# Kernel tuning notes

Measured on AMD Instinct MI355X. Metric: run time of the kernel, lower is better.

## Reference

```python
import jax, jax.numpy as jnp
import numpy as np

EPS = 1e-6        # module eps added to softplus(sigma)
BALL_EPS = 1e-5   # clip margin for Poincare ball projection


def _norm(x):
    return jnp.sqrt(jnp.clip(jnp.sum(x * x, axis=-1, keepdims=True), 1e-15))


def _clip_norm(x, max_norm):
    n = _norm(x)
    return x * jnp.minimum(1.0, max_norm / n)


def _artanh(x):
    return jnp.arctanh(jnp.clip(x, -1.0 + 1e-7, 1.0 - 1e-7))


def _expmap0(u, c):
    """pre_clip -> PoincareBall.expmap0 -> post_clip."""
    sc = jnp.sqrt(c)
    max_tan = jnp.arctanh(jnp.asarray(1.0 - BALL_EPS, u.dtype)) / sc
    u = _clip_norm(u, max_tan)                      # pre_clip on tangent norm
    n = _norm(u)
    y = jnp.tanh(sc * n) * u / (sc * n)
    return _clip_norm(y, (1.0 - BALL_EPS) / sc)     # post_clip inside ball


def _logmap0(y, c):
    sc = jnp.sqrt(c)
    n = _norm(y)
    return _artanh(sc * n) * y / (sc * n)


def _pair_dist(qh, kh, c):
    """Poincare distance d(q_i, k_j) computed from inner products (no [B,H,N,J,D] tensor).
    qh: (B,H,N,D), kh: (B,H,J,D) -> (B,H,N,J).
    d = (2/sqrt(c)) * artanh(sqrt(c) * ||(-q) mobius_add k||).
    """
    x2 = jnp.sum(qh * qh, -1)[..., :, None]   # (B,H,N,1)
    y2 = jnp.sum(kh * kh, -1)[..., None, :]   # (B,H,1,J)
    xy = jnp.einsum('bhnd,bhjd->bhnj', qh, kh)
    A = 1.0 - 2.0 * c * xy + c * y2
    Bc = 1.0 - c * x2
    num2 = A * A * x2 - 2.0 * A * Bc * xy + Bc * Bc * y2   # ||numerator||^2
    den = 1.0 - 2.0 * c * xy + (c * c) * x2 * y2
    arg = jnp.sqrt(c) * jnp.sqrt(jnp.clip(num2, 0.0)) / jnp.clip(den, 1e-15)
    return (2.0 / jnp.sqrt(c)) * _artanh(arg)


def _mobius_scalar_mul(r, x, c):
    sc = jnp.sqrt(c)
    n = _norm(x)
    return jnp.tanh(r * _artanh(sc * n)) * x / (sc * n)


def setup_inputs() -> dict:
    key = jax.random.key(0)
    ks = jax.random.split(key, 8)
    B, N, D, H, M = 16, 576, 768, 12, 128
    Hd = D // H
    std = 0.02
    isp1 = float(np.log(np.expm1(1.0)))  # inv_softplus(1.0)
    return {
        'x': jax.random.normal(ks[0], (B, N, D), jnp.float32),
        'Wq': jax.random.normal(ks[1], (D, D), jnp.float32) * std,
        'bq': jnp.zeros((D,), jnp.float32),
        'Wk': jax.random.normal(ks[2], (D, D), jnp.float32) * std,
        'bk': jnp.zeros((D,), jnp.float32),
        'Wv': jax.random.normal(ks[3], (D, D), jnp.float32) * std,
        'bv': jnp.zeros((D,), jnp.float32),
        'Wo': jax.random.normal(ks[4], (D, D), jnp.float32) * std,
        'bo': jnp.zeros((D,), jnp.float32),
        'centroids': jax.random.normal(ks[5], (H, M, Hd), jnp.float32) * std,
        'curv_raw': jnp.full((1,), isp1, jnp.float32),
        'sigma_raw': jnp.full((H,), isp1, jnp.float32),
    }


def reference(x, Wq, bq, Wk, bk, Wv, bv, Wo, bo, centroids, curv_raw, sigma_raw):
    B, N, D = x.shape
    H, M, Hd = centroids.shape
    c = jax.nn.softplus(curv_raw[0])

    def split(t):  # (B,N,D) -> (B,H,N,Hd)
        return t.reshape(B, N, H, Hd).transpose(0, 2, 1, 3)

    q = split(x @ Wq.T + bq)
    k = split(x @ Wk.T + bk)
    v = split(x @ Wv.T + bv)

    Cb = jnp.broadcast_to(centroids[None], (B, H, M, Hd))
    K_aug = jnp.concatenate([k, Cb], axis=2)   # (B,H,J,Hd), J = N + M
    V_aug = jnp.concatenate([v, Cb], axis=2)

    q_h = _expmap0(q, c)
    K_h = _expmap0(K_aug, c)
    V_h = _expmap0(V_aug, c)

    d = _pair_dist(q_h, K_h, c)                              # (B,H,N,J)
    sigma = (jax.nn.softplus(sigma_raw) + EPS)[None, :, None, None]
    W = jax.nn.softmax(-(d * d) / (2.0 * sigma * sigma), axis=-1)

    # Riemannian weighted midpoint (geoopt weighted_midpoint with k=-c):
    # gamma = lambda_x = 2 / (1 - c||x||^2)
    gamma = 2.0 / jnp.clip(1.0 - c * jnp.sum(V_h * V_h, -1), 1e-15)  # (B,H,J)
    nom = jnp.einsum('bhnj,bhjd->bhnd', W * gamma[:, :, None, :], V_h)
    den = jnp.einsum('bhnj,bhj->bhn', W, gamma - 1.0)
    den = jnp.where(den >= 0, jnp.maximum(den, 1e-10), jnp.minimum(den, -1e-10))
    two_mean = nom / den[..., None]
    O_h = _mobius_scalar_mul(0.5, two_mean, c)
    O_euc = _logmap0(O_h, c)                                  # (B,H,N,Hd)

    out = O_euc.transpose(0, 2, 1, 3).reshape(B, N, H * Hd)
    return out @ Wo.T + bo
```

## Files before the change

### kernel.cpp

```cpp
#include <hip/hip_runtime.h>
#include <cstdint>
#include <cstddef>

#define B_  16
#define N_  576
#define D_  768
#define H_  12
#define HD_ 64
#define M_  128
#define J_  704

typedef unsigned short u16;
typedef __attribute__((ext_vector_type(8))) short bf16x8;
typedef __attribute__((ext_vector_type(4))) float f32x4;
typedef __attribute__((ext_vector_type(4))) unsigned short u16x4;
typedef __attribute__((ext_vector_type(8))) unsigned short u16x8;


__device__ __forceinline__ float softplus_f(float x) {
    return (x > 20.f) ? x : log1pf(expf(x));
}

__device__ __forceinline__ float wred_sum64(float v) {
#pragma unroll
    for (int m = 1; m < 64; m <<= 1) v += __shfl_xor(v, m, 64);
    return v;
}

__device__ __forceinline__ u16 bf16_rne(float f) {
    unsigned int u = __float_as_uint(f);
    unsigned int r = u + 0x7FFFu + ((u >> 16) & 1u);
    return (u16)(r >> 16);
}
__device__ __forceinline__ float bf16_tof(u16 h) {
    return __uint_as_float(((unsigned int)h) << 16);
}

__device__ __forceinline__ float expmap0_factor(float n2, float sc, float* n2out) {
    const float ATANH_1M1E5 = 6.1030335f;
    float n0 = sqrtf(fmaxf(n2, 1e-15f));
    float maxtan = ATANH_1M1E5 / sc;
    float f1 = fminf(1.f, maxtan / n0);
    float n1 = n0 * f1;
    float a  = sc * n1;
    float th = tanhf(a);
    float yfac  = th / a;
    float ynorm = th / sc;
    float lim   = (1.f - 1e-5f) / sc;
    float f2 = fminf(1.f, lim / ynorm);
    float fn = ynorm * f2;
    *n2out = fn * fn;
    return f1 * yfac * f2;
}

__device__ __forceinline__ float artanh_fast(float z) {
    return 0.5f * __logf((1.f + z) / (1.f - z));
}

typedef const __attribute__((address_space(1))) unsigned int* gas_u32;
typedef __attribute__((address_space(3))) unsigned int* las_u32;
__device__ __forceinline__ void gload_lds16(const u16* g, u16* l) {
    __builtin_amdgcn_global_load_lds((gas_u32)(const void*)g, (las_u32)(void*)l, 16, 0, 0);
}

__global__ __launch_bounds__(256) void split_bf16_kernel(
    const float* __restrict__ src, u16* __restrict__ hi, u16* __restrict__ lo, int n4)
{
    int i = blockIdx.x * 256 + threadIdx.x;
    if (i >= n4) return;
    float4 v = ((const float4*)src)[i];
    u16x4 h, l;
    h[0] = bf16_rne(v.x); l[0] = bf16_rne(v.x - bf16_tof(h[0]));
    h[1] = bf16_rne(v.y); l[1] = bf16_rne(v.y - bf16_tof(h[1]));
    h[2] = bf16_rne(v.z); l[2] = bf16_rne(v.z - bf16_tof(h[2]));
    h[3] = bf16_rne(v.w); l[3] = bf16_rne(v.w - bf16_tof(h[3]));
    ((u16x4*)hi)[i] = h;
    ((u16x4*)lo)[i] = l;
}

__global__ __launch_bounds__(256) void split_w4_kernel(
    const float* __restrict__ W0, const float* __restrict__ W1,
    const float* __restrict__ W2, const float* __restrict__ W3,
    u16* __restrict__ H0, u16* __restrict__ L0, u16* __restrict__ H1, u16* __restrict__ L1,
    u16* __restrict__ H2, u16* __restrict__ L2, u16* __restrict__ H3, u16* __restrict__ L3)
{
    int i = blockIdx.x * 256 + threadIdx.x;
    const int wsel = blockIdx.y;
    const float* src = wsel == 0 ? W0 : (wsel == 1 ? W1 : (wsel == 2 ? W2 : W3));
    u16* hi = wsel == 0 ? H0 : (wsel == 1 ? H1 : (wsel == 2 ? H2 : H3));
    u16* lo = wsel == 0 ? L0 : (wsel == 1 ? L1 : (wsel == 2 ? L2 : L3));
    float4 v = ((const float4*)src)[i];
    u16x4 h, l;
    h[0] = bf16_rne(v.x); l[0] = bf16_rne(v.x - bf16_tof(h[0]));
    h[1] = bf16_rne(v.y); l[1] = bf16_rne(v.y - bf16_tof(h[1]));
    h[2] = bf16_rne(v.z); l[2] = bf16_rne(v.z - bf16_tof(h[2]));
    h[3] = bf16_rne(v.w); l[3] = bf16_rne(v.w - bf16_tof(h[3]));
    ((u16x4*)hi)[i] = h;
    ((u16x4*)lo)[i] = l;
}

__global__ __launch_bounds__(256) void gemm_qkv_mfma(
    const u16* __restrict__ xh, const u16* __restrict__ xl,
    const u16* __restrict__ Wh0, const u16* __restrict__ Wl0,
    const u16* __restrict__ Wh1, const u16* __restrict__ Wl1,
    const u16* __restrict__ Wh2, const u16* __restrict__ Wl2,
    const float* __restrict__ bq, const float* __restrict__ bk, const float* __restrict__ bv,
    float* __restrict__ qh_o, float* __restrict__ Kh_o, float* __restrict__ Vh_o)
{
    __shared__ u16 Ah[4096], Al[4096], Bh[4096], Bl[4096];
    const int tid = threadIdx.x;
    const int w = tid >> 6, lane = tid & 63;
    const int wr = w >> 1, wc = w & 1;
    const int lrow = lane & 15, lk8 = (lane >> 4) << 3;
    const int bid = blockIdx.x;
    const int xcd = bid & 7, ser = bid >> 3;
    const int mt = xcd * 9 + (ser % 9);
    const int yb = ser / 9;
    const int which = yb / 6, ct = yb - which * 6;
    const u16* Bp_h = which == 0 ? Wh0 : (which == 1 ? Wh1 : Wh2);
    const u16* Bp_l = which == 0 ? Wl0 : (which == 1 ? Wl1 : Wl2);
    const int row0 = mt * 128, col0 = ct * 128;

    const size_t a0 = (size_t)(row0 + (2 * w + 0) * 16 + lrow) * 768 + lk8;
    const size_t a1 = a0 + 16 * 768;
    const size_t b0 = (size_t)(col0 + (2 * w + 0) * 16 + lrow) * 768 + lk8;
    const size_t b1 = b0 + 16 * 768;
    u16* lAh0 = Ah + (2 * w) * 512; u16* lAh1 = lAh0 + 512;
    u16* lAl0 = Al + (2 * w) * 512; u16* lAl1 = lAl0 + 512;
    u16* lBh0 = Bh + (2 * w) * 512; u16* lBh1 = lBh0 + 512;
    u16* lBl0 = Bl + (2 * w) * 512; u16* lBl1 = lBl0 + 512;

    f32x4 acc[4][4];
#pragma unroll
    for (int i = 0; i < 4; ++i)
#pragma unroll
        for (int j = 0; j < 4; ++j) acc[i][j] = (f32x4){0.f, 0.f, 0.f, 0.f};

    for (int k0 = 0; k0 < 768; k0 += 32) {
        gload_lds16(xh + a0 + k0, lAh0);
        gload_lds16(xh + a1 + k0, lAh1);
        gload_lds16(xl + a0 + k0, lAl0);
        gload_lds16(xl + a1 + k0, lAl1);
        gload_lds16(Bp_h + b0 + k0, lBh0);
        gload_lds16(Bp_h + b1 + k0, lBh1);
        gload_lds16(Bp_l + b0 + k0, lBl0);
        gload_lds16(Bp_l + b1 + k0, lBl1);
        __syncthreads();
        bf16x8 aH[4], aL[4], bH[4], bL[4];
        const int lo8 = lane * 8;
#pragma unroll
        for (int i = 0; i < 4; ++i) {
            aH[i] = *(const bf16x8*)(Ah + (wr * 4 + i) * 512 + lo8);
            aL[i] = *(const bf16x8*)(Al + (wr * 4 + i) * 512 + lo8);
            bH[i] = *(const bf16x8*)(Bh + (wc * 4 + i) * 512 + lo8);
            bL[i] = *(const bf16x8*)(Bl + (wc * 4 + i) * 512 + lo8);
        }
#pragma unroll
        for (int mi = 0; mi < 4; ++mi)
#pragma unroll
            for (int ni = 0; ni < 4; ++ni) {
                acc[mi][ni] = __builtin_amdgcn_mfma_f32_16x16x32_bf16(aH[mi], bH[ni], acc[mi][ni], 0, 0, 0);
                acc[mi][ni] = __builtin_amdgcn_mfma_f32_16x16x32_bf16(aH[mi], bL[ni], acc[mi][ni], 0, 0, 0);
                acc[mi][ni] = __builtin_amdgcn_mfma_f32_16x16x32_bf16(aL[mi], bH[ni], acc[mi][ni], 0, 0, 0);
            }
        __syncthreads();
    }

    const float* bias = which == 0 ? bq : (which == 1 ? bk : bv);
    const int h = ct * 2 + wc;
    const int rbase = row0 + wr * 64 + ((lane >> 4) << 2);
#pragma unroll
    for (int ni = 0; ni < 4; ++ni) {
        const int hd = ni * 16 + lrow;
        const float bv_ = bias[h * 64 + hd];
#pragma unroll
        for (int mi = 0; mi < 4; ++mi) {
            f32x4 a = acc[mi][ni];
#pragma unroll
            for (int r = 0; r < 4; ++r) {
                int row = rbase + mi * 16 + r;
                int bb = row / 576;
                int nn = row - bb * 576;
                float val = a[r] + bv_;
                size_t dst = (((size_t)(bb * 12 + h)) * 576 + nn) * 64 + hd;
                if (which == 0)      qh_o[dst] = val;
                else if (which == 1) Kh_o[dst] = val;
                else                 Vh_o[dst] = val;
            }
        }
    }
}

__global__ __launch_bounds__(256) void gemm_o_mfma(
    const u16* __restrict__ Oh, const u16* __restrict__ Ol,
    const u16* __restrict__ Wh, const u16* __restrict__ Wl,
    const float* __restrict__ bo, float* __restrict__ out)
{
    __shared__ u16 Ah[4096], Al[4096], Bh[4096], Bl[4096];
    const int tid = threadIdx.x;
    const int w = tid >> 6, lane = tid & 63;
    const int wr = w >> 1, wc = w & 1;
    const int lrow = lane & 15, lk8 = (lane >> 4) << 3;
    const int bid = blockIdx.x;
    const int xcd = bid & 7, ser = bid >> 3;
    const int mt = xcd * 9 + (ser % 9);
    const int ct = ser / 9;
    const int row0 = mt * 128, col0 = ct * 128;

    const size_t a0 = (size_t)(row0 + (2 * w + 0) * 16 + lrow) * 768 + lk8;
    const size_t a1 = a0 + 16 * 768;
    const size_t b0 = (size_t)(col0 + (2 * w + 0) * 16 + lrow) * 768 + lk8;
    const size_t b1 = b0 + 16 * 768;
    u16* lAh0 = Ah + (2 * w) * 512; u16* lAh1 = lAh0 + 512;
    u16* lAl0 = Al + (2 * w) * 512; u16* lAl1 = lAl0 + 512;
    u16* lBh0 = Bh + (2 * w) * 512; u16* lBh1 = lBh0 + 512;
    u16* lBl0 = Bl + (2 * w) * 512; u16* lBl1 = lBl0 + 512;

    f32x4 acc[4][4];
#pragma unroll
    for (int i = 0; i < 4; ++i)
#pragma unroll
        for (int j = 0; j < 4; ++j) acc[i][j] = (f32x4){0.f, 0.f, 0.f, 0.f};

    for (int k0 = 0; k0 < 768; k0 += 32) {
        gload_lds16(Oh + a0 + k0, lAh0);
        gload_lds16(Oh + a1 + k0, lAh1);
        gload_lds16(Ol + a0 + k0, lAl0);
        gload_lds16(Ol + a1 + k0, lAl1);
        gload_lds16(Wh + b0 + k0, lBh0);
        gload_lds16(Wh + b1 + k0, lBh1);
        gload_lds16(Wl + b0 + k0, lBl0);
        gload_lds16(Wl + b1 + k0, lBl1);
        __syncthreads();
        bf16x8 aH[4], aL[4], bH[4], bL[4];
        const int lo8 = lane * 8;
#pragma unroll
        for (int i = 0; i < 4; ++i) {
            aH[i] = *(const bf16x8*)(Ah + (wr * 4 + i) * 512 + lo8);
            aL[i] = *(const bf16x8*)(Al + (wr * 4 + i) * 512 + lo8);
            bH[i] = *(const bf16x8*)(Bh + (wc * 4 + i) * 512 + lo8);
            bL[i] = *(const bf16x8*)(Bl + (wc * 4 + i) * 512 + lo8);
        }
#pragma unroll
        for (int mi = 0; mi < 4; ++mi)
#pragma unroll
            for (int ni = 0; ni < 4; ++ni) {
                acc[mi][ni] = __builtin_amdgcn_mfma_f32_16x16x32_bf16(aH[mi], bH[ni], acc[mi][ni], 0, 0, 0);
                acc[mi][ni] = __builtin_amdgcn_mfma_f32_16x16x32_bf16(aH[mi], bL[ni], acc[mi][ni], 0, 0, 0);
                acc[mi][ni] = __builtin_amdgcn_mfma_f32_16x16x32_bf16(aL[mi], bH[ni], acc[mi][ni], 0, 0, 0);
            }
        __syncthreads();
    }

    const int rbase = row0 + wr * 64 + ((lane >> 4) << 2);
#pragma unroll
    for (int ni = 0; ni < 4; ++ni) {
        const int colg = col0 + wc * 64 + ni * 16 + lrow;
        const float bv_ = bo[colg];
#pragma unroll
        for (int mi = 0; mi < 4; ++mi) {
            f32x4 a = acc[mi][ni];
#pragma unroll
            for (int r = 0; r < 4; ++r) {
                int row = rbase + mi * 16 + r;
                out[(size_t)row * 768 + colg] = a[r] + bv_;
            }
        }
    }
}

__global__ __launch_bounds__(256) void maps_kernel(
    const float* __restrict__ qh, const float* __restrict__ Khf, const float* __restrict__ Vhf,
    const float* __restrict__ cent,
    u16* __restrict__ Qb0, u16* __restrict__ Qb1, u16* __restrict__ Qb2,
    u16* __restrict__ Kb0, u16* __restrict__ Kb1, u16* __restrict__ Kb2,
    u16* __restrict__ Kc0, u16* __restrict__ Kc1, u16* __restrict__ Kc2,
    u16* __restrict__ gV0, u16* __restrict__ gV1,
    u16* __restrict__ gVc0, u16* __restrict__ gVc1,
    float* __restrict__ x2q, float* __restrict__ y2g, float* __restrict__ gm1,
    float* __restrict__ y2c, float* __restrict__ gm1c,
    const float* __restrict__ curv_raw)
{
    __shared__ float gvt_s[64][65];
    const float c  = softplus_f(curv_raw[0]);
    const float sc = sqrtf(c);
    const int bx = blockIdx.x;
    const int w = threadIdx.x >> 6, lane = threadIdx.x & 63;

    if (bx < 1728) {
        const size_t base = (size_t)bx * 64;
#pragma unroll 4
        for (int i = 0; i < 16; ++i) {
            const size_t row = base + w * 16 + i;
            const size_t off = row * 64 + lane;
            float u = qh[off];
            float n2 = wred_sum64(u * u);
            float n2o;
            float f = expmap0_factor(n2, sc, &n2o);
            float y = u * f;
            u16 h_ = bf16_rne(y);
            float r1 = y - bf16_tof(h_);
            u16 m_ = bf16_rne(r1);
            u16 l_ = bf16_rne(r1 - bf16_tof(m_));
            Qb0[off] = h_; Qb1[off] = m_; Qb2[off] = l_;
            if (lane == 0) x2q[row] = n2o;
        }
        return;
    }
    if (bx < 3456) {
        const int t = bx - 1728;
        const int bh = t / 9, jt = t - (t / 9) * 9;
#pragma unroll 4
        for (int i = 0; i < 16; ++i) {
            const int j = jt * 64 + w * 16 + i;
            const size_t g = (size_t)bh * 576 + j;
            float kx = Khf[g * 64 + lane], vx = Vhf[g * 64 + lane];
            float n2k = wred_sum64(kx * kx);
            float n2v = wred_sum64(vx * vx);
            float y2o, v2o;
            float fk = expmap0_factor(n2k, sc, &y2o);
            float fv = expmap0_factor(n2v, sc, &v2o);
            float ky = kx * fk;
            u16 kh = bf16_rne(ky);
            float r1 = ky - bf16_tof(kh);
            u16 km = bf16_rne(r1);
            u16 kl = bf16_rne(r1 - bf16_tof(km));
            Kb0[g * 64 + lane] = kh; Kb1[g * 64 + lane] = km; Kb2[g * 64 + lane] = kl;
            float gmm = 2.f / fmaxf(1.f - c * v2o, 1e-15f);
            gvt_s[lane][w * 16 + i] = vx * fv * gmm;
            if (lane == 0) { y2g[g] = y2o; gm1[g] = gmm - 1.f; }
        }
        __syncthreads();
        const int hd = threadIdx.x >> 2, j0 = (threadIdx.x & 3) * 16;
        u16 hb[16], lb[16];
#pragma unroll
        for (int e = 0; e < 16; ++e) {
            float v = gvt_s[hd][j0 + e];
            hb[e] = bf16_rne(v);
            lb[e] = bf16_rne(v - bf16_tof(hb[e]));
        }
        const size_t dst = ((size_t)bh * 64 + hd) * 576 + jt * 64 + j0;
        *(u16x8*)(gV0 + dst)     = *(u16x8*)&hb[0];
        *(u16x8*)(gV0 + dst + 8) = *(u16x8*)&hb[8];
        *(u16x8*)(gV1 + dst)     = *(u16x8*)&lb[0];
        *(u16x8*)(gV1 + dst + 8) = *(u16x8*)&lb[8];
        return;
    }
    {
        const int t = bx - 3456;
        const int h = t >> 1, ct = t & 1;
#pragma unroll 4
        for (int i = 0; i < 16; ++i) {
            const int m = ct * 64 + w * 16 + i;
            const size_t g = (size_t)h * 128 + m;
            float cv = cent[g * 64 + lane];
            float n2 = wred_sum64(cv * cv);
            float n2o;
            float f = expmap0_factor(n2, sc, &n2o);
            float ky = cv * f;
            u16 kh = bf16_rne(ky);
            float r1 = ky - bf16_tof(kh);
            u16 km = bf16_rne(r1);
            u16 kl = bf16_rne(r1 - bf16_tof(km));
            Kc0[g * 64 + lane] = kh; Kc1[g * 64 + lane] = km; Kc2[g * 64 + lane] = kl;
            float gmm = 2.f / fmaxf(1.f - c * n2o, 1e-15f);
            gvt_s[lane][w * 16 + i] = ky * gmm;
            if (lane == 0) { y2c[g] = n2o; gm1c[g] = gmm - 1.f; }
        }
        __syncthreads();
        const int hd = threadIdx.x >> 2, j0 = (threadIdx.x & 3) * 16;
        u16 hb[16], lb[16];
#pragma unroll
        for (int e = 0; e < 16; ++e) {
            float v = gvt_s[hd][j0 + e];
            hb[e] = bf16_rne(v);
            lb[e] = bf16_rne(v - bf16_tof(hb[e]));
        }
        const size_t dst = ((size_t)h * 64 + hd) * 128 + ct * 64 + j0;
        *(u16x8*)(gVc0 + dst)     = *(u16x8*)&hb[0];
        *(u16x8*)(gVc0 + dst + 8) = *(u16x8*)&hb[8];
        *(u16x8*)(gVc1 + dst)     = *(u16x8*)&lb[0];
        *(u16x8*)(gVc1 + dst + 8) = *(u16x8*)&lb[8];
    }
}

__global__ __launch_bounds__(256) void attn_kernel(
    const u16* __restrict__ Qb0, const u16* __restrict__ Qb1, const u16* __restrict__ Qb2,
    const u16* __restrict__ Kb0, const u16* __restrict__ Kb1, const u16* __restrict__ Kb2,
    const u16* __restrict__ Kc0, const u16* __restrict__ Kc1, const u16* __restrict__ Kc2,
    const u16* __restrict__ gV0, const u16* __restrict__ gV1,
    const u16* __restrict__ gVc0, const u16* __restrict__ gVc1,
    const float* __restrict__ x2q, const float* __restrict__ y2g, const float* __restrict__ gm1,
    const float* __restrict__ y2c, const float* __restrict__ gm1c,
    const float* __restrict__ sigma_raw, const float* __restrict__ curv_raw,
    u16* __restrict__ Oh, u16* __restrict__ Ol)
{
    __shared__ __align__(16) u16 Kst[2][3][4096];
    __shared__ __align__(16) u16 Vst[2][4096];
    __shared__ __align__(16) u16 wb_hi[4][1024];
    __shared__ __align__(16) u16 wb_lo[4][1024];

    const int blk = blockIdx.x;
    const int xcd = blk & 7;
    const int serial = blk >> 3;
    const int bhg = serial / 9;
    const int qt = serial - bhg * 9;
    const int bh = bhg * 8 + xcd;
    const int b = bh / 12, h = bh % 12;
    const float c  = softplus_f(curv_raw[0]);
    const float sc = sqrtf(c);
    const float sig = softplus_f(sigma_raw[h]) + 1e-6f;
    const float coef = -2.f / (c * sig * sig);
    const float c2h  = coef * 0.25f * 0.6931471805599453f;
    const float m2c  = -2.f * c;
    const float CLIP = 1.f - 1e-7f;

    const int tid = threadIdx.x;
    const int w = tid >> 6, lane = tid & 63;
    const int lr = lane & 15, lg = lane >> 4, lo8 = lg * 8;
    const int swl = (lr & 7) << 3;

    const size_t qbase = (size_t)bh * 576 + qt * 64;

    int srow[2], scol[2];
#pragma unroll
    for (int rr = 0; rr < 2; ++rr) {
        int cch = (rr * 4 + w) * 64 + lane;
        srow[rr] = cch >> 3;
        scol[rr] = ((cch & 7) ^ (srow[rr] & 7)) << 3;
    }
    const size_t kb_base = (size_t)bh * 576 * 64;
    const size_t kc_base = (size_t)h * 128 * 64;
    const size_t vb_base = (size_t)bh * 64 * 576;
    const size_t vc_base = (size_t)h * 64 * 128;

    auto stageK = [&](int t, int buf) {
        if (t < 9) {
            const size_t rb = kb_base + (size_t)t * 64 * 64;
#pragma unroll
            for (int rr = 0; rr < 2; ++rr) {
                const size_t so = rb + (size_t)srow[rr] * 64 + scol[rr];
                gload_lds16(Kb0 + so, &Kst[buf][0][(rr * 4 + w) * 512]);
                gload_lds16(Kb1 + so, &Kst[buf][1][(rr * 4 + w) * 512]);
                gload_lds16(Kb2 + so, &Kst[buf][2][(rr * 4 + w) * 512]);
            }
        } else {
            const size_t rb = kc_base + (size_t)(t - 9) * 64 * 64;
#pragma unroll
            for (int rr = 0; rr < 2; ++rr) {
                const size_t so = rb + (size_t)srow[rr] * 64 + scol[rr];
                gload_lds16(Kc0 + so, &Kst[buf][0][(rr * 4 + w) * 512]);
                gload_lds16(Kc1 + so, &Kst[buf][1][(rr * 4 + w) * 512]);
                gload_lds16(Kc2 + so, &Kst[buf][2][(rr * 4 + w) * 512]);
            }
        }
    };
    auto stageV = [&](int t) {
        if (t < 9) {
            const size_t rb = vb_base + (size_t)t * 64;
#pragma unroll
            for (int rr = 0; rr < 2; ++rr) {
                const size_t so = rb + (size_t)srow[rr] * 576 + scol[rr];
                gload_lds16(gV0 + so, &Vst[0][(rr * 4 + w) * 512]);
                gload_lds16(gV1 + so, &Vst[1][(rr * 4 + w) * 512]);
            }
        } else {
            const size_t rb = vc_base + (size_t)(t - 9) * 64;
#pragma unroll
            for (int rr = 0; rr < 2; ++rr) {
                const size_t so = rb + (size_t)srow[rr] * 128 + scol[rr];
                gload_lds16(gVc0 + so, &Vst[0][(rr * 4 + w) * 512]);
                gload_lds16(gVc1 + so, &Vst[1][(rr * 4 + w) * 512]);
            }
        }
    };

    bf16x8 aQh[2], aQm[2], aQl[2];
    {
        const size_t qrow = (qbase + w * 16 + lr) * 64;
#pragma unroll
        for (int kt = 0; kt < 2; ++kt) {
            const size_t o = qrow + kt * 32 + lo8;
            aQh[kt] = *(const bf16x8*)(Qb0 + o);
            aQm[kt] = *(const bf16x8*)(Qb1 + o);
            aQl[kt] = *(const bf16x8*)(Qb2 + o);
        }
    }
    float x2r[4], m2Bc[4], Bc2[4], ccx2[4];
#pragma unroll
    for (int r = 0; r < 4; ++r) {
        float x2 = x2q[qbase + w * 16 + lg * 4 + r];
        float Bc = fmaf(-c, x2, 1.f);
        x2r[r] = x2; m2Bc[r] = -2.f * Bc; Bc2[r] = Bc * Bc; ccx2[r] = c * c * x2;
    }

    f32x4 pv[4];
#pragma unroll
    for (int i = 0; i < 4; ++i) pv[i] = (f32x4){0.f, 0.f, 0.f, 0.f};
    float den[4] = {0.f, 0.f, 0.f, 0.f};

    u16* wbh = &wb_hi[w][0];
    u16* wbl = &wb_lo[w][0];

    stageK(0, 0);
    __syncthreads();

    int cur = 0;
    for (int jt = 0; jt < 11; ++jt) {
        const int jb = jt * 64;

        if (jt < 10) stageK(jt + 1, cur ^ 1);
        stageV(jt);

        const float* y2p;
        const float* gm1p;
        if (jt < 9) { y2p = y2g + (size_t)bh * 576 + jb;  gm1p = gm1 + (size_t)bh * 576 + jb; }
        else        { y2p = y2c + (size_t)h * 128 + (jb - 576); gm1p = gm1c + (size_t)h * 128 + (jb - 576); }

        const u16* kp0 = &Kst[cur][0][0];
        const u16* kp1 = &Kst[cur][1][0];
        const u16* kp2 = &Kst[cur][2][0];
        f32x4 sf[4];
        float y2v[4], gm1v[4];
#pragma unroll
        for (int jf = 0; jf < 4; ++jf) {
            y2v[jf] = y2p[jf * 16 + lr];
            gm1v[jf] = gm1p[jf * 16 + lr];
            const int rb = (jf * 16 + lr) * 64;
            f32x4 s = (f32x4){0.f, 0.f, 0.f, 0.f};
#pragma unroll
            for (int kt = 0; kt < 2; ++kt) {
                const int o = rb + ((kt * 32 + lo8) ^ swl);
                bf16x8 kh = *(const bf16x8*)(kp0 + o);
                bf16x8 km = *(const bf16x8*)(kp1 + o);
                bf16x8 kl = *(const bf16x8*)(kp2 + o);
                s = __builtin_amdgcn_mfma_f32_16x16x32_bf16(aQh[kt], kh, s, 0, 0, 0);
                s = __builtin_amdgcn_mfma_f32_16x16x32_bf16(aQh[kt], km, s, 0, 0, 0);
                s = __builtin_amdgcn_mfma_f32_16x16x32_bf16(aQm[kt], kh, s, 0, 0, 0);
                s = __builtin_amdgcn_mfma_f32_16x16x32_bf16(aQm[kt], km, s, 0, 0, 0);
                s = __builtin_amdgcn_mfma_f32_16x16x32_bf16(aQh[kt], kl, s, 0, 0, 0);
                s = __builtin_amdgcn_mfma_f32_16x16x32_bf16(aQl[kt], kh, s, 0, 0, 0);
            }
            sf[jf] = s;
        }

#pragma unroll
        for (int jf = 0; jf < 4; ++jf) {
            const float y2 = y2v[jf];
            const float cy2 = c * y2;
#pragma unroll
            for (int r = 0; r < 4; ++r) {
                float xy = sf[jf][r];
                float one = fmaf(m2c, xy, 1.f);
                float A   = one + cy2;
                float dn  = fmaf(ccx2[r], y2, one);
                float u   = A * x2r[r];
                u = fmaf(m2Bc[r], xy, u);
                float num2 = fmaf(A, u, Bc2[r] * y2);
                num2 = fmaxf(num2, 0.f);
                float s = sqrtf(num2) * sc;
                float dnc = fmaxf(dn, 1e-15f);
                s = fminf(s, dnc * CLIP);
                float td = __builtin_amdgcn_logf(dnc + s) - __builtin_amdgcn_logf(dnc - s);
                float wv_ = __builtin_amdgcn_exp2f(c2h * td * td);
                sf[jf][r] = wv_;
                den[r] = fmaf(wv_, gm1v[jf], den[r]);
            }
        }

#pragma unroll
        for (int r = 0; r < 4; ++r) {
            const int row = lg * 4 + r;
            const int sw = (row & 7) << 3;
#pragma unroll
            for (int jf = 0; jf < 4; ++jf) {
                const int colu = (jf * 16 + lr) ^ sw;
                float wv_ = sf[jf][r];
                u16 hb = bf16_rne(wv_);
                wbh[row * 64 + colu] = hb;
                wbl[row * 64 + colu] = bf16_rne(wv_ - bf16_tof(hb));
            }
        }

        __syncthreads();

        bf16x8 aWh[2], aWl[2];
#pragma unroll
        for (int kt = 0; kt < 2; ++kt) {
            const int colu = (kt * 32 + lo8) ^ swl;
            aWh[kt] = *(const bf16x8*)(wbh + lr * 64 + colu);
            aWl[kt] = *(const bf16x8*)(wbl + lr * 64 + colu);
        }

#pragma unroll
        for (int hf = 0; hf < 4; ++hf) {
            const int rb = (hf * 16 + lr) * 64;
#pragma unroll
            for (int kt = 0; kt < 2; ++kt) {
                const int o = rb + ((kt * 32 + lo8) ^ swl);
                bf16x8 vh = *(const bf16x8*)(&Vst[0][o]);
                bf16x8 vl = *(const bf16x8*)(&Vst[1][o]);
                pv[hf] = __builtin_amdgcn_mfma_f32_16x16x32_bf16(aWh[kt], vh, pv[hf], 0, 0, 0);
                pv[hf] = __builtin_amdgcn_mfma_f32_16x16x32_bf16(aWh[kt], vl, pv[hf], 0, 0, 0);
                pv[hf] = __builtin_amdgcn_mfma_f32_16x16x32_bf16(aWl[kt], vh, pv[hf], 0, 0, 0);
            }
        }

        __syncthreads();
        cur ^= 1;
    }

#pragma unroll
    for (int r = 0; r < 4; ++r) {
        float d = den[r];
#pragma unroll
        for (int msk = 1; msk < 16; msk <<= 1) d += __shfl_xor(d, msk, 64);
        float rd = 1.f / d;
        float o_[4];
        float n2 = 0.f;
#pragma unroll
        for (int hf = 0; hf < 4; ++hf) { o_[hf] = pv[hf][r] * rd; n2 = fmaf(o_[hf], o_[hf], n2); }
#pragma unroll
        for (int msk = 1; msk < 16; msk <<= 1) n2 += __shfl_xor(n2, msk, 64);
        float nrm = sqrtf(fmaxf(n2, 1e-15f));
        float arg = fminf(sc * nrm, 1.f - 1e-7f);
        float t = artanh_fast(arg);
        float f = 0.5f * t / (sc * nrm);
        const int nrow = qt * 64 + w * 16 + lg * 4 + r;
        const size_t dst = ((size_t)(b * 576 + nrow)) * 768 + h * 64;
#pragma unroll
        for (int hf = 0; hf < 4; ++hf) {
            float val = o_[hf] * f;
            u16 hb = bf16_rne(val);
            Oh[dst + hf * 16 + lr] = hb;
            Ol[dst + hf * 16 + lr] = bf16_rne(val - bf16_tof(hb));
        }
    }
}

extern "C" void kernel_launch(void* const* d_in, const int* in_sizes, int n_in,
                              void* d_out, int out_size, void* d_ws, size_t ws_size,
                              hipStream_t stream) {
    (void)in_sizes; (void)n_in; (void)out_size; (void)ws_size;
    const float* x    = (const float*)d_in[0];
    const float* Wq   = (const float*)d_in[1];
    const float* bq   = (const float*)d_in[2];
    const float* Wk   = (const float*)d_in[3];
    const float* bk   = (const float*)d_in[4];
    const float* Wv   = (const float*)d_in[5];
    const float* bv   = (const float*)d_in[6];
    const float* Wo   = (const float*)d_in[7];
    const float* bo   = (const float*)d_in[8];
    const float* cent = (const float*)d_in[9];
    const float* curv = (const float*)d_in[10];
    const float* sigr = (const float*)d_in[11];
    float* out = (float*)d_out;

    const size_t QH  = (size_t)B_ * H_ * N_ * 64;
    const size_t CK  = (size_t)H_ * M_ * 64;
    const size_t WSZ = (size_t)D_ * D_;

    float* fp = (float*)d_ws;
    float* qh   = fp;            fp += QH;
    float* Khf  = fp;            fp += QH;
    float* Vhf  = fp;            fp += QH;
    float* x2q  = fp;            fp += (size_t)B_ * H_ * N_;
    float* y2g  = fp;            fp += (size_t)B_ * H_ * N_;
    float* gm1  = fp;            fp += (size_t)B_ * H_ * N_;
    float* y2c  = fp;            fp += (size_t)H_ * M_;
    float* gm1c = fp;            fp += (size_t)H_ * M_;
    u16* up = (u16*)fp;
    u16* xh  = up;  up += QH;
    u16* xl  = up;  up += QH;
    u16* Oh  = xh;
    u16* Ol  = xl;
    u16* Wqh = up;  up += WSZ;
    u16* Wql = up;  up += WSZ;
    u16* Wkh = up;  up += WSZ;
    u16* Wkl = up;  up += WSZ;
    u16* Wvh = up;  up += WSZ;
    u16* Wvl = up;  up += WSZ;
    u16* Woh = up;  up += WSZ;
    u16* Wol = up;  up += WSZ;
    u16* Qb  = up;  up += 3 * QH;
    u16* Kb  = up;  up += 3 * QH;
    u16* gV  = up;  up += 2 * QH;
    u16* Kc  = up;  up += 3 * CK;
    u16* gVc = up;  up += 2 * CK;

    u16* Qb0 = Qb;           u16* Qb1 = Qb + QH;   u16* Qb2 = Qb + 2 * QH;
    u16* Kb0 = Kb;           u16* Kb1 = Kb + QH;   u16* Kb2 = Kb + 2 * QH;
    u16* gV0 = gV;           u16* gV1 = gV + QH;
    u16* Kc0 = Kc;           u16* Kc1 = Kc + CK;   u16* Kc2 = Kc + 2 * CK;
    u16* gVc0 = gVc;         u16* gVc1 = gVc + CK;

    split_bf16_kernel<<<(int)(QH / 4 / 256), 256, 0, stream>>>(x, xh, xl, (int)(QH / 4));
    split_w4_kernel<<<dim3((int)(WSZ / 4 / 256), 4), 256, 0, stream>>>(
        Wq, Wk, Wv, Wo, Wqh, Wql, Wkh, Wkl, Wvh, Wvl, Woh, Wol);

    gemm_qkv_mfma<<<1296, 256, 0, stream>>>(xh, xl, Wqh, Wql, Wkh, Wkl, Wvh, Wvl,
                                            bq, bk, bv, qh, Khf, Vhf);
    maps_kernel<<<3480, 256, 0, stream>>>(qh, Khf, Vhf, cent,
                                          Qb0, Qb1, Qb2, Kb0, Kb1, Kb2, Kc0, Kc1, Kc2,
                                          gV0, gV1, gVc0, gVc1,
                                          x2q, y2g, gm1, y2c, gm1c, curv);
    attn_kernel<<<1728, 256, 0, stream>>>(Qb0, Qb1, Qb2, Kb0, Kb1, Kb2, Kc0, Kc1, Kc2,
                                          gV0, gV1, gVc0, gVc1,
                                          x2q, y2g, gm1, y2c, gm1c, sigr, curv, Oh, Ol);
    gemm_o_mfma<<<432, 256, 0, stream>>>(Oh, Ol, Woh, Wol, bo, out);
}
```

Measured before the change: 458.7 us.

## Fuse expmap0 and bf16 splitting into QKV GEMM epilogue, drop maps kernel

The QKV GEMM epilogue now computes per-row norms with lane shuffles across the MFMA tile, applies the expmap0 factor, and writes the multi-bf16 split Q/K and gamma-scaled transposed V directly, along with the per-row scalars. This removes the fp32 q/K/V intermediates and the separate maps kernel's read/write pass. Centroid processing moves to a small standalone kernel. In exchange the epilogue does more arithmetic and issues scattered 2-byte stores for Q/K, which may be poorly coalesced.

```diff
diff --git a/kernel.cpp b/kernel.cpp
--- a/kernel.cpp
+++ b/kernel.cpp
@@ -105,7 +105,11 @@
     const u16* __restrict__ Wh1, const u16* __restrict__ Wl1,
     const u16* __restrict__ Wh2, const u16* __restrict__ Wl2,
     const float* __restrict__ bq, const float* __restrict__ bk, const float* __restrict__ bv,
-    float* __restrict__ qh_o, float* __restrict__ Kh_o, float* __restrict__ Vh_o)
+    u16* __restrict__ Qb0, u16* __restrict__ Qb1, u16* __restrict__ Qb2,
+    u16* __restrict__ Kb0, u16* __restrict__ Kb1, u16* __restrict__ Kb2,
+    u16* __restrict__ gV0, u16* __restrict__ gV1,
+    float* __restrict__ x2q, float* __restrict__ y2g, float* __restrict__ gm1,
+    const float* __restrict__ curv_raw)
 {
     __shared__ u16 Ah[4096], Al[4096], Bh[4096], Bl[4096];
     const int tid = threadIdx.x;
@@ -169,23 +173,84 @@
     const float* bias = which == 0 ? bq : (which == 1 ? bk : bv);
     const int h = ct * 2 + wc;
     const int rbase = row0 + wr * 64 + ((lane >> 4) << 2);
-#pragma unroll
-    for (int ni = 0; ni < 4; ++ni) {
-        const int hd = ni * 16 + lrow;
-        const float bv_ = bias[h * 64 + hd];
-#pragma unroll
-        for (int mi = 0; mi < 4; ++mi) {
+    const float c  = softplus_f(curv_raw[0]);
+    const float sc = sqrtf(c);
+    float bvv[4];
+#pragma unroll
+    for (int ni = 0; ni < 4; ++ni) bvv[ni] = bias[h * 64 + ni * 16 + lrow];
+
+#pragma unroll
+    for (int mi = 0; mi < 4; ++mi) {
+        float v4[4][4];
+#pragma unroll
+        for (int ni = 0; ni < 4; ++ni) {
             f32x4 a = acc[mi][ni];
 #pragma unroll
-            for (int r = 0; r < 4; ++r) {
-                int row = rbase + mi * 16 + r;
-                int bb = row / 576;
-                int nn = row - bb * 576;
-                float val = a[r] + bv_;
-                size_t dst = (((size_t)(bb * 12 + h)) * 576 + nn) * 64 + hd;
-                if (which == 0)      qh_o[dst] = val;
-                else if (which == 1) Kh_o[dst] = val;
-                else                 Vh_o[dst] = val;
+            for (int r = 0; r < 4; ++r) v4[ni][r] = a[r] + bvv[ni];
+        }
+        float f_[4], n2o_[4];
+#pragma unroll
+        for (int r = 0; r < 4; ++r) {
+            float p[4];
+#pragma unroll
+            for (int ni = 0; ni < 4; ++ni) {
+                float s = v4[ni][r] * v4[ni][r];
+#pragma unroll
+                for (int m = 1; m < 16; m <<= 1) s += __shfl_xor(s, m, 64);
+                p[ni] = s;
+            }
+            float n2 = (p[0] + p[1]) + (p[2] + p[3]);
+            f_[r] = expmap0_factor(n2, sc, &n2o_[r]);
+        }
+        const int row0g = rbase + mi * 16;
+        const int bb = row0g / 576;
+        const int nn0 = row0g - bb * 576;
+        const size_t gbase = ((size_t)(bb * 12 + h)) * 576 + nn0;
+        if (which == 2) {
+            float gmm[4];
+#pragma unroll
+            for (int r = 0; r < 4; ++r) gmm[r] = 2.f / fmaxf(1.f - c * n2o_[r], 1e-15f);
+            if (lrow == 0) {
+#pragma unroll
+                for (int r = 0; r < 4; ++r) gm1[gbase + r] = gmm[r] - 1.f;
+            }
+#pragma unroll
+            for (int ni = 0; ni < 4; ++ni) {
+                const int hd = ni * 16 + lrow;
+                u16x4 hs, ls;
+#pragma unroll
+                for (int r = 0; r < 4; ++r) {
+                    float gv = v4[ni][r] * f_[r] * gmm[r];
+                    u16 hb = bf16_rne(gv);
+                    hs[r] = hb;
+                    ls[r] = bf16_rne(gv - bf16_tof(hb));
+                }
+                const size_t dst = (((size_t)(bb * 12 + h)) * 64 + hd) * 576 + nn0;
+                *(u16x4*)(gV0 + dst) = hs;
+                *(u16x4*)(gV1 + dst) = ls;
+            }
+        } else {
+            float* scal = which == 0 ? x2q : y2g;
+            if (lrow == 0) {
+#pragma unroll
+                for (int r = 0; r < 4; ++r) scal[gbase + r] = n2o_[r];
+            }
+            u16* P0 = which == 0 ? Qb0 : Kb0;
+            u16* P1 = which == 0 ? Qb1 : Kb1;
+            u16* P2 = which == 0 ? Qb2 : Kb2;
+#pragma unroll
+            for (int ni = 0; ni < 4; ++ni) {
+                const int hd = ni * 16 + lrow;
+#pragma unroll
+                for (int r = 0; r < 4; ++r) {
+                    float y = v4[ni][r] * f_[r];
+                    u16 hb = bf16_rne(y);
+                    float r1 = y - bf16_tof(hb);
+                    u16 mb = bf16_rne(r1);
+                    u16 lb = bf16_rne(r1 - bf16_tof(mb));
+                    const size_t off = (gbase + r) * 64 + hd;
+                    P0[off] = hb; P1[off] = mb; P2[off] = lb;
+                }
             }
         }
     }
@@ -269,119 +334,51 @@
     }
 }
 
-__global__ __launch_bounds__(256) void maps_kernel(
-    const float* __restrict__ qh, const float* __restrict__ Khf, const float* __restrict__ Vhf,
+__global__ __launch_bounds__(256) void cent_kernel(
     const float* __restrict__ cent,
-    u16* __restrict__ Qb0, u16* __restrict__ Qb1, u16* __restrict__ Qb2,
-    u16* __restrict__ Kb0, u16* __restrict__ Kb1, u16* __restrict__ Kb2,
     u16* __restrict__ Kc0, u16* __restrict__ Kc1, u16* __restrict__ Kc2,
-    u16* __restrict__ gV0, u16* __restrict__ gV1,
     u16* __restrict__ gVc0, u16* __restrict__ gVc1,
-    float* __restrict__ x2q, float* __restrict__ y2g, float* __restrict__ gm1,
     float* __restrict__ y2c, float* __restrict__ gm1c,
     const float* __restrict__ curv_raw)
 {
     __shared__ float gvt_s[64][65];
     const float c  = softplus_f(curv_raw[0]);
     const float sc = sqrtf(c);
-    const int bx = blockIdx.x;
+    const int t = blockIdx.x;
+    const int h = t >> 1, ct = t & 1;
     const int w = threadIdx.x >> 6, lane = threadIdx.x & 63;
-
-    if (bx < 1728) {
-        const size_t base = (size_t)bx * 64;
 #pragma unroll 4
-        for (int i = 0; i < 16; ++i) {
-            const size_t row = base + w * 16 + i;
-            const size_t off = row * 64 + lane;
-            float u = qh[off];
-            float n2 = wred_sum64(u * u);
-            float n2o;
-            float f = expmap0_factor(n2, sc, &n2o);
-            float y = u * f;
-            u16 h_ = bf16_rne(y);
-            float r1 = y - bf16_tof(h_);
-            u16 m_ = bf16_rne(r1);
-            u16 l_ = bf16_rne(r1 - bf16_tof(m_));
-            Qb0[off] = h_; Qb1[off] = m_; Qb2[off] = l_;
-            if (lane == 0) x2q[row] = n2o;
-        }
-        return;
-    }
-    if (bx < 3456) {
-        const int t = bx - 1728;
-        const int bh = t / 9, jt = t - (t / 9) * 9;
-#pragma unroll 4
-        for (int i = 0; i < 16; ++i) {
-            const int j = jt * 64 + w * 16 + i;
-            const size_t g = (size_t)bh * 576 + j;
-            float kx = Khf[g * 64 + lane], vx = Vhf[g * 64 + lane];
-            float n2k = wred_sum64(kx * kx);
-            float n2v = wred_sum64(vx * vx);
-            float y2o, v2o;
-            float fk = expmap0_factor(n2k, sc, &y2o);
-            float fv = expmap0_factor(n2v, sc, &v2o);
-            float ky = kx * fk;
-            u16 kh = bf16_rne(ky);
-            float r1 = ky - bf16_tof(kh);
-            u16 km = bf16_rne(r1);
-            u16 kl = bf16_rne(r1 - bf16_tof(km));
-            Kb0[g * 64 + lane] = kh; Kb1[g * 64 + lane] = km; Kb2[g * 64 + lane] = kl;
-            float gmm = 2.f / fmaxf(1.f - c * v2o, 1e-15f);
-            gvt_s[lane][w * 16 + i] = vx * fv * gmm;
-            if (lane == 0) { y2g[g] = y2o; gm1[g] = gmm - 1.f; }
-        }
-        __syncthreads();
-        const int hd = threadIdx.x >> 2, j0 = (threadIdx.x & 3) * 16;
-        u16 hb[16], lb[16];
-#pragma unroll
-        for (int e = 0; e < 16; ++e) {
-            float v = gvt_s[hd][j0 + e];
-            hb[e] = bf16_rne(v);
-            lb[e] = bf16_rne(v - bf16_tof(hb[e]));
-        }
-        const size_t dst = ((size_t)bh * 64 + hd) * 576 + jt * 64 + j0;
-        *(u16x8*)(gV0 + dst)     = *(u16x8*)&hb[0];
-        *(u16x8*)(gV0 + dst + 8) = *(u16x8*)&hb[8];
-        *(u16x8*)(gV1 + dst)     = *(u16x8*)&lb[0];
-        *(u16x8*)(gV1 + dst + 8) = *(u16x8*)&lb[8];
-        return;
-    }
-    {
-        const int t = bx - 3456;
-        const int h = t >> 1, ct = t & 1;
-#pragma unroll 4
-        for (int i = 0; i < 16; ++i) {
-            const int m = ct * 64 + w * 16 + i;
-            const size_t g = (size_t)h * 128 + m;
-            float cv = cent[g * 64 + lane];
-            float n2 = wred_sum64(cv * cv);
-            float n2o;
-            float f = expmap0_factor(n2, sc, &n2o);
-            float ky = cv * f;
-            u16 kh = bf16_rne(ky);
-            float r1 = ky - bf16_tof(kh);
-            u16 km = bf16_rne(r1);
-            u16 kl = bf16_rne(r1 - bf16_tof(km));
-            Kc0[g * 64 + lane] = kh; Kc1[g * 64 + lane] = km; Kc2[g * 64 + lane] = kl;
-            float gmm = 2.f / fmaxf(1.f - c * n2o, 1e-15f);
-            gvt_s[lane][w * 16 + i] = ky * gmm;
-            if (lane == 0) { y2c[g] = n2o; gm1c[g] = gmm - 1.f; }
-        }
-        __syncthreads();
-        const int hd = threadIdx.x >> 2, j0 = (threadIdx.x & 3) * 16;
-        u16 hb[16], lb[16];
-#pragma unroll
-        for (int e = 0; e < 16; ++e) {
-            float v = gvt_s[hd][j0 + e];
-            hb[e] = bf16_rne(v);
-            lb[e] = bf16_rne(v - bf16_tof(hb[e]));
-        }
-        const size_t dst = ((size_t)h * 64 + hd) * 128 + ct * 64 + j0;
-        *(u16x8*)(gVc0 + dst)     = *(u16x8*)&hb[0];
-        *(u16x8*)(gVc0 + dst + 8) = *(u16x8*)&hb[8];
-        *(u16x8*)(gVc1 + dst)     = *(u16x8*)&lb[0];
-        *(u16x8*)(gVc1 + dst + 8) = *(u16x8*)&lb[8];
-    }
+    for (int i = 0; i < 16; ++i) {
+        const int m = ct * 64 + w * 16 + i;
+        const size_t g = (size_t)h * 128 + m;
+        float cv = cent[g * 64 + lane];
+        float n2 = wred_sum64(cv * cv);
+        float n2o;
+        float f = expmap0_factor(n2, sc, &n2o);
+        float ky = cv * f;
+        u16 kh = bf16_rne(ky);
+        float r1 = ky - bf16_tof(kh);
+        u16 km = bf16_rne(r1);
+        u16 kl = bf16_rne(r1 - bf16_tof(km));
+        Kc0[g * 64 + lane] = kh; Kc1[g * 64 + lane] = km; Kc2[g * 64 + lane] = kl;
+        float gmm = 2.f / fmaxf(1.f - c * n2o, 1e-15f);
+        gvt_s[lane][w * 16 + i] = ky * gmm;
+        if (lane == 0) { y2c[g] = n2o; gm1c[g] = gmm - 1.f; }
+    }
+    __syncthreads();
+    const int hd = threadIdx.x >> 2, j0 = (threadIdx.x & 3) * 16;
+    u16 hb[16], lb[16];
+#pragma unroll
+    for (int e = 0; e < 16; ++e) {
+        float v = gvt_s[hd][j0 + e];
+        hb[e] = bf16_rne(v);
+        lb[e] = bf16_rne(v - bf16_tof(hb[e]));
+    }
+    const size_t dst = ((size_t)h * 64 + hd) * 128 + ct * 64 + j0;
+    *(u16x8*)(gVc0 + dst)     = *(u16x8*)&hb[0];
+    *(u16x8*)(gVc0 + dst + 8) = *(u16x8*)&hb[8];
+    *(u16x8*)(gVc1 + dst)     = *(u16x8*)&lb[0];
+    *(u16x8*)(gVc1 + dst + 8) = *(u16x8*)&lb[8];
 }
 
 __global__ __launch_bounds__(256) void attn_kernel(
@@ -661,9 +658,6 @@
     const size_t WSZ = (size_t)D_ * D_;
 
     float* fp = (float*)d_ws;
-    float* qh   = fp;            fp += QH;
-    float* Khf  = fp;            fp += QH;
-    float* Vhf  = fp;            fp += QH;
     float* x2q  = fp;            fp += (size_t)B_ * H_ * N_;
     float* y2g  = fp;            fp += (size_t)B_ * H_ * N_;
     float* gm1  = fp;            fp += (size_t)B_ * H_ * N_;
@@ -698,12 +692,12 @@
     split_w4_kernel<<<dim3((int)(WSZ / 4 / 256), 4), 256, 0, stream>>>(
         Wq, Wk, Wv, Wo, Wqh, Wql, Wkh, Wkl, Wvh, Wvl, Woh, Wol);
 
+    cent_kernel<<<24, 256, 0, stream>>>(cent, Kc0, Kc1, Kc2, gVc0, gVc1, y2c, gm1c, curv);
+
     gemm_qkv_mfma<<<1296, 256, 0, stream>>>(xh, xl, Wqh, Wql, Wkh, Wkl, Wvh, Wvl,
-                                            bq, bk, bv, qh, Khf, Vhf);
-    maps_kernel<<<3480, 256, 0, stream>>>(qh, Khf, Vhf, cent,
-                                          Qb0, Qb1, Qb2, Kb0, Kb1, Kb2, Kc0, Kc1, Kc2,
-                                          gV0, gV1, gVc0, gVc1,
-                                          x2q, y2g, gm1, y2c, gm1c, curv);
+                                            bq, bk, bv,
+                                            Qb0, Qb1, Qb2, Kb0, Kb1, Kb2, gV0, gV1,
+                                            x2q, y2g, gm1, curv);
     attn_kernel<<<1728, 256, 0, stream>>>(Qb0, Qb1, Qb2, Kb0, Kb1, Kb2, Kc0, Kc1, Kc2,
                                           gV0, gV1, gVc0, gVc1,
                                           x2q, y2g, gm1, y2c, gm1c, sigr, curv, Oh, Ol);
```

Measured after the change: 430.3 us. 1.07x faster.
